# Optimization experiments

Measured on AMD Instinct MI355X. Metric: run time of the kernel, lower is better.

Reference implementation:

```python
import jax, jax.numpy as jnp
import numpy as np

GROUP = 16   # self.group
K = 3        # self.k (top-3 motif rows)


def _unfold3(x):
    # nn.Unfold(kernel_size=3): [B,C,H,W] -> [B, C*9, (H-2)*(W-2)]
    # torch channel ordering: c-major, then kernel offsets row-major.
    B, C, H, W = x.shape
    Ho, Wo = H - 2, W - 2
    pats = jnp.stack([x[:, :, i:i + Ho, j:j + Wo]
                      for i in range(3) for j in range(3)], axis=2)  # [B,C,9,Ho,Wo]
    return pats.reshape(B, C * 9, Ho * Wo)


def _fold3(y, H, W):
    # nn.Fold(output_size=(H,W), kernel_size=3): sum overlapping patches back.
    B, C9, L = y.shape
    C = C9 // 9
    Ho, Wo = H - 2, W - 2
    y = y.reshape(B, C, 3, 3, Ho, Wo)
    out = jnp.zeros((B, C, H, W), y.dtype)
    for i in range(3):
        for j in range(3):
            out = out.at[:, :, i:i + Ho, j:j + Wo].add(y[:, :, i, j])
    return out


def _group_motif(xg, H, W):
    motif = _unfold3(xg)                                  # [B,P,L], P = Cg*9
    B, P, L = motif.shape
    # torch.cdist (p=2) between the P rows, via the Gram trick.
    sq = jnp.sum(motif * motif, axis=-1)                  # [B,P]
    gram = jnp.einsum('bpl,bql->bpq', motif, motif)       # [B,P,P]
    d2 = sq[:, :, None] + sq[:, None, :] - 2.0 * gram
    dist = jnp.sqrt(jnp.maximum(d2, 0.0))
    eye = jnp.eye(P, dtype=bool)[None]
    dist = jnp.where(eye, jnp.inf, dist)                  # diagonal := inf
    # topk(k=1, largest=False) == argmin over last dim
    min_idx = jnp.argmin(dist, axis=-1)                   # [B,P] int
    # torch.unique(return_counts=True) over the whole tensor (flattened over batch)
    counts = jnp.bincount(min_idx.ravel(), length=P)      # [P] int
    # sort counts descending, take first K uniques -> lax.top_k
    top_c, top_i = jax.lax.top_k(counts, K)               # [K],[K]
    total = jnp.sum(top_c).astype(motif.dtype)
    rows = motif[:, top_i, :]                             # [B,K,L] gathered motif rows
    cf = top_c.astype(motif.dtype)
    motif_new = jnp.zeros_like(motif)
    for o in range(K):
        # torch: motif * motif[:, u_o].unsqueeze(1) * c_o // total  (floor division)
        motif_new = motif_new + jnp.floor(motif * rows[:, o][:, None, :] * cf[o] / total)
    return _fold3(motif_new, H, W)


def setup_inputs() -> dict:
    key = jax.random.key(0)
    feature = jax.random.normal(key, (2, 256, 192, 192), dtype=jnp.float32)
    return {"feature": feature}


def reference(feature):
    B, C, H, W = feature.shape
    chunks = jnp.split(feature, GROUP, axis=1)
    outs = [_group_motif(g, H, W) for g in chunks]
    return jnp.concatenate(outs, axis=1)                  # [B, C, H, W]
```

## Files before the change

kernel.cpp:

```cpp
#include <hip/hip_runtime.h>
#include <math.h>

#define NB 2
#define NC 256
#define CG 16
#define HH 192
#define WW 192
#define HO 190
#define PP 144

typedef float v2f __attribute__((ext_vector_type(2)));

#define SMEM_FLOATS 7348

#define GLD16(GP, LP)                                                         \
    __builtin_amdgcn_global_load_lds(                                         \
        (const __attribute__((address_space(1))) void*)(GP),                  \
        (__attribute__((address_space(3))) void*)(LP), 16, 0, 0)

__global__ __launch_bounds__(192, 2) void gram_kernel(const float* __restrict__ x,
                                                      double* __restrict__ gram)
{
    __shared__ __align__(16) float smem[SMEM_FLOATS];
    float* const red_s = smem + 2548;

    const int v = threadIdx.x;
    const int p = v & 1;
    const int bb = (v + 2) & ~1;

    const int bid = blockIdx.x;
    const int vx = bid & 7;
    const int tq = bid >> 3;
    const int idxw = tq / 36;
    const int rr0 = tq - idxw * 36;
    const int hg = idxw * 8 + vx;
    const int bg = hg >> 1;
    int r = rr0 + 36 * (hg & 1);
    int c2 = 0;
    while (r >= (c2 + 2) / 2) { r -= (c2 + 2) / 2; ++c2; }
    const int c1a = 2 * r;
    int c1b = 2 * r + 1;
    const bool bval = (c1b <= c2);
    if (!bval) c1b = c2;
    const int b = bg >> 4, g = bg & 15;

    const float* __restrict__ xa  = x + ((size_t)(b * NC + g * CG + c1a)) * (HH * WW);
    const float* __restrict__ xb  = x + ((size_t)(b * NC + g * CG + c1b)) * (HH * WW);
    const float* __restrict__ x2g = x + ((size_t)(b * NC + g * CG + c2 )) * (HH * WW);

    v2f midA[15], midB[15];
#pragma unroll
    for (int o = 0; o < 15; ++o) { midA[o] = (v2f){0.f, 0.f}; midB[o] = (v2f){0.f, 0.f}; }

    v2f win[6][3];
    float ca[6], cb[6];
#pragma unroll
    for (int k = 0; k < 6; ++k) {
        ca[k] = xa[(size_t)(2 + k) * WW + v];
        cb[k] = xb[(size_t)(2 + k) * WW + v];
    }

    const float* pa = xa + (size_t)8 * WW + v;
    const float* pb = xb + (size_t)8 * WW + v;
    int lds_off;

#define USTEP6(P, WPF, GPF)                                                   \
    {                                                                         \
        const float a1 = ca[(P)];                                             \
        const float b1 = cb[(P)];                                             \
        if (GPF) { ca[(P)] = pa[(P) * WW]; cb[(P)] = pb[(P) * WW]; }          \
        if (WPF) {                                                            \
            _Pragma("unroll")                                                 \
            for (int pr = 0; pr < 3; ++pr)                                    \
                win[((P) + 5) % 6][pr] = *(const v2f*)(&smem[lds_off + 2 * pr]); \
        }                                                                     \
        lds_off += 196;                                                       \
        const v2f a2 = (v2f){a1, a1};                                         \
        const v2f b2 = (v2f){b1, b1};                                         \
        _Pragma("unroll")                                                     \
        for (int kk = 0; kk < 5; ++kk) {                                      \
            _Pragma("unroll")                                                 \
            for (int pr = 0; pr < 3; ++pr) {                                  \
                const v2f wv = win[((P) + kk) % 6][pr];                       \
                midA[kk * 3 + pr] = __builtin_elementwise_fma(a2, wv, midA[kk * 3 + pr]); \
                midB[kk * 3 + pr] = __builtin_elementwise_fma(b2, wv, midB[kk * 3 + pr]); \
            }                                                                 \
        }                                                                     \
    }

#define STAGE(ROW0, NROUND, LASTN)                                            \
    __syncthreads();                                                          \
    _Pragma("unroll")                                                         \
    for (int rr2 = 0; rr2 < (NROUND); ++rr2) {                                \
        if (rr2 < (NROUND) - 1 || v < (LASTN)) {                              \
            const int slot = rr2 * 192 + v;                                   \
            const int row = slot / 49;                                        \
            const int s49 = slot - row * 49;                                  \
            const int col = (s49 == 0) ? 0 : (s49 - 1) * 4;                   \
            const float* gp2 = x2g + (size_t)((ROW0) + row) * WW + col;       \
            float* lp = smem + (rr2 * 192 + (v & ~63)) * 4;                   \
            GLD16(gp2, lp);                                                   \
        }                                                                     \
    }                                                                         \
    __syncthreads();                                                          \
    if (v < 144) smem[(v >> 2) * 196 + (v & 3)] = 0.f;                        \
    __syncthreads();

    for (int band = 0; band < 6; ++band) {
        const int row0 = band * 30;
        STAGE(row0, 9, 179)

        if (band == 0) {
#pragma unroll
            for (int k = 0; k < 5; ++k)
#pragma unroll
            for (int pr = 0; pr < 3; ++pr)
                win[k][pr] = *(const v2f*)(&smem[k * 196 + bb + 2 * pr]);
        }

        lds_off = 5 * 196 + bb;
        for (int it = 0; it < 5; ++it) {
            USTEP6(0, 1, 1) USTEP6(1, 1, 1) USTEP6(2, 1, 1)
            USTEP6(3, 1, 1) USTEP6(4, 1, 1) USTEP6(5, 1, 1)
            pa += 6 * WW; pb += 6 * WW;
        }
    }
    STAGE(180, 4, 12)
    lds_off = 5 * 196 + bb;
    USTEP6(0, 1, 1) USTEP6(1, 1, 1) USTEP6(2, 1, 0)
    USTEP6(3, 1, 0) USTEP6(4, 1, 0) USTEP6(5, 1, 0)
    USTEP6(0, 1, 0) USTEP6(1, 0, 0)
#undef USTEP6
#undef STAGE

    __syncthreads();
    for (int i = 0; i < 12; ++i) {
        const int ar = (i < 6) ? (i - 2) : (188 + i - 6);
        const float val = (ar >= 0 && ar <= 191) ? x2g[(size_t)ar * WW + v] : 0.f;
        smem[i * 196 + 4 + v] = val;
    }
    __syncthreads();

    double* const gp = gram + (size_t)bg * (PP * PP);

#pragma unroll
    for (int i1 = 0; i1 < 3; ++i1) {
        const int ra = (i1 == 0) ? 0 : ((i1 == 1) ? 1 : 190);
        const int rb = (i1 == 0) ? 1 : ((i1 == 1) ? 190 : 191);
#pragma unroll
        for (int c = 0; c < 2; ++c) {
            const float* __restrict__ xc = (c == 0) ? xa : xb;
            const float xra = xc[(size_t)ra * WW + v];
            const float xrb = xc[(size_t)rb * WW + v];
#pragma unroll
            for (int k = 0; k < 5; ++k) {
                const int bufa = (ra < 2) ? (ra + k) : (ra + k - 184);
                const int bufb = (rb < 2) ? (rb + k) : (rb + k - 184);
#pragma unroll
                for (int dj = 0; dj < 5; ++dj) {
                    float ve, vo;
                    {
                        const int pr = dj >> 1, ln = dj & 1;
                        const v2f m = (c == 0) ? midA[k * 3 + pr] : midB[k * 3 + pr];
                        ve = ln ? m.y : m.x;
                    }
                    {
                        const int pr = (dj + 1) >> 1, ln = (dj + 1) & 1;
                        const v2f m = (c == 0) ? midA[k * 3 + pr] : midB[k * 3 + pr];
                        vo = ln ? m.y : m.x;
                    }
                    float cw = p ? vo : ve;
                    cw = fmaf(xra, smem[bufa * 196 + 2 + v + dj], cw);
                    cw = fmaf(xrb, smem[bufb * 196 + 2 + v + dj], cw);
                    red_s[v * 25 + k * 5 + dj] = cw;
                }
            }
            __syncthreads();
            float e0 = 0.f, e1 = 0.f, e190 = 0.f, e191 = 0.f;
            if (v < 25) {
                e0   = red_s[0 * 25 + v];
                e1   = red_s[1 * 25 + v];
                e190 = red_s[190 * 25 + v];
                e191 = red_s[191 * 25 + v];
            }
            __syncthreads();
#pragma unroll
            for (int s = 96; s >= 3; s >>= 1) {
                for (int idx = v; idx < s * 25; idx += 192) {
                    const int vv = idx / 25, o = idx - vv * 25;
                    red_s[vv * 25 + o] += red_s[(vv + s) * 25 + o];
                }
                __syncthreads();
            }
            if (v < 25 && (c == 0 || bval)) {
                const int di = v / 5 - 2, dj = v - (v / 5) * 5 - 2;
                const int i2 = i1 + di;
                if (i2 >= 0 && i2 <= 2) {
                    const float S = red_s[0 * 25 + v] + red_s[1 * 25 + v] + red_s[2 * 25 + v];
                    const int c1 = (c == 0) ? c1a : c1b;
#pragma unroll
                    for (int j1 = 0; j1 < 3; ++j1) {
                        const int j2 = j1 + dj;
                        if (j2 < 0 || j2 > 2) continue;
                        const float W = S - ((j1 == 0) ? (e190 + e191)
                                          : (j1 == 1) ? (e0 + e191)
                                                      : (e0 + e1));
                        const int pp = c1 * 9 + i1 * 3 + j1;
                        const int qq = c2 * 9 + i2 * 3 + j2;
                        gp[pp * PP + qq] = (double)W;
                        if (c1 != c2) gp[qq * PP + pp] = (double)W;
                    }
                }
            }
            __syncthreads();
        }
    }
}

__global__ __launch_bounds__(320) void topk_kernel(const double* __restrict__ gram,
                                                   float* __restrict__ pf,
                                                   int* __restrict__ pi)
{
    const int g = blockIdx.x;
    __shared__ double sdiag[2][PP];
    __shared__ int counts[PP];
    const int tid = threadIdx.x;
    if (tid < PP) counts[tid] = 0;
    if (tid < 2 * PP) {
        const int b = tid / PP, p = tid % PP;
        const double* gb = gram + (size_t)(b * 16 + g) * (PP * PP);
        sdiag[b][p] = gb[p * PP + p];
    }
    __syncthreads();
    if (tid < 2 * PP) {
        const int b = tid / PP, p = tid % PP;
        const double* row = gram + ((size_t)(b * 16 + g) * PP + p) * PP;
        const double sp = sdiag[b][p];
        double best = 1e300;
        int bi = 0;
        for (int q = 0; q < PP; ++q) {
            if (q == p) continue;
            const double d2 = sp + sdiag[b][q] - 2.0 * row[q];
            if (d2 < best) { best = d2; bi = q; }
        }
        atomicAdd(&counts[bi], 1);
    }
    __syncthreads();
    if (tid == 0) {
        int sel[3], cv[3];
        for (int o = 0; o < 3; ++o) {
            int bc = -1, bp = 0;
            for (int p = 0; p < PP; ++p) {
                bool taken = false;
                for (int u = 0; u < o; ++u) if (sel[u] == p) taken = true;
                if (!taken && counts[p] > bc) { bc = counts[p]; bp = p; }
            }
            sel[o] = bp; cv[o] = bc;
        }
        const int tot = cv[0] + cv[1] + cv[2];
        for (int o = 0; o < 3; ++o) {
            pf[g * 4 + o] = (float)cv[o];
            pi[g * 4 + o] = sel[o];
        }
        pf[g * 4 + 3] = (float)tot;
    }
}

template <bool EDGE>
__device__ __forceinline__ void motif_quad(const float* __restrict__ x,
                                           const float* __restrict__ pf,
                                           const int* __restrict__ pi,
                                           float* __restrict__ out,
                                           int b, int ch, int h, int w0)
{
    const int g = ch >> 4;
    const size_t base = ((size_t)(b * NC + ch)) * (HH * WW);
    const float4 xv4 = *(const float4*)(x + base + (size_t)h * WW + w0);
    const float xs[4] = {xv4.x, xv4.y, xv4.z, xv4.w};
    float acc[4] = {0.f, 0.f, 0.f, 0.f};
    const float total = pf[g * 4 + 3];
    const double invd = 1.0 / (double)total;

#pragma unroll
    for (int o = 0; o < 3; ++o) {
        const int p = pi[g * 4 + o];
        const float cff = pf[g * 4 + o];
        const int co = p / 9;
        const int kk = p - co * 9;
        const int io = kk / 3, jo = kk - (kk / 3) * 3;
        const float* Rb = x + ((size_t)(b * NC + g * CG + co)) * (HH * WW);
#pragma unroll
        for (int i = 0; i < 3; ++i) {
            const int ho = h - i;
            bool rowok = true;
            int hr = ho + io;
            if (EDGE) {
                rowok = (ho >= 0) && (ho < HO);
                hr = hr < 0 ? 0 : (hr > HH - 1 ? HH - 1 : hr);
            }
            const float* row = Rb + (size_t)hr * WW;
            float rv[6];
#pragma unroll
            for (int u = 0; u < 6; ++u) {
                int col = w0 - 2 + jo + u;
                if (EDGE) col = col < 0 ? 0 : (col > WW - 1 ? WW - 1 : col);
                rv[u] = row[col];
            }
#pragma unroll
            for (int j = 0; j < 3; ++j)
#pragma unroll
            for (int q = 0; q < 4; ++q) {
                const float r2 = rv[q - j + 2];
                const float t1 = xs[q] * r2;
                const float t2 = t1 * cff;
                const float qf = (float)((double)t2 * invd);
                const float vfl = floorf(qf);
                if (EDGE) {
                    const int wo = w0 + q - j;
                    const bool ok = rowok && (wo >= 0) && (wo < HO);
                    acc[q] += ok ? vfl : 0.f;
                } else {
                    acc[q] += vfl;
                }
            }
        }
    }
    float4 ov = make_float4(acc[0], acc[1], acc[2], acc[3]);
    *(float4*)(out + base + (size_t)h * WW + w0) = ov;
}

__global__ __launch_bounds__(256) void out_interior(const float* __restrict__ x,
                                                    const float* __restrict__ pf,
                                                    const int* __restrict__ pi,
                                                    float* __restrict__ out)
{
    const int gid = blockIdx.x * 256 + threadIdx.x;
    const int w4i = gid % 46;
    int t = gid / 46;
    const int h = 2 + t % 188; t /= 188;
    const int ch = t & 255;
    const int b = t >> 8;
    motif_quad<false>(x, pf, pi, out, b, ch, h, (w4i + 1) * 4);
}

__global__ __launch_bounds__(256) void out_edge(const float* __restrict__ x,
                                                const float* __restrict__ pf,
                                                const int* __restrict__ pi,
                                                float* __restrict__ out)
{
    const int gid = blockIdx.x * 256 + threadIdx.x;
    const int e = gid % 568;
    int t = gid / 568;
    const int ch = t & 255;
    const int b = t >> 8;
    int h, w4;
    if (e < 192) {
        const int hs = e / 48;
        h = (hs < 2) ? hs : 188 + hs;
        w4 = e % 48;
    } else {
        const int e2 = e - 192;
        h = 2 + (e2 >> 1);
        w4 = (e2 & 1) ? 47 : 0;
    }
    motif_quad<true>(x, pf, pi, out, b, ch, h, w4 * 4);
}

extern "C" void kernel_launch(void* const* d_in, const int* in_sizes, int n_in,
                              void* d_out, int out_size, void* d_ws, size_t ws_size,
                              hipStream_t stream)
{
    const float* x = (const float*)d_in[0];
    float* out = (float*)d_out;

    double* gram = (double*)d_ws;
    const size_t gram_bytes = (size_t)32 * PP * PP * sizeof(double);
    float* pf = (float*)((char*)d_ws + gram_bytes);
    int* pi = (int*)((char*)d_ws + gram_bytes + 256);

    gram_kernel<<<2304, 192, 0, stream>>>(x, gram);
    topk_kernel<<<16, 320, 0, stream>>>(gram, pf, pi);
    out_interior<<<17296, 256, 0, stream>>>(x, pf, pi, out);
    out_edge<<<1136, 256, 0, stream>>>(x, pf, pi, out);
}
```

Baseline: 364.1 us.

## Shrink gram LDS footprint, fold reduction, merge output kernels, float-divide via FMA refinement

The gram kernel stages smaller 24-row bands so its LDS buffer is smaller, and pre-folds the 192-entry epilogue reduction into 96 slots with edge values kept in a separate small buffer. The aim is to let more blocks fit per CU and cut one reduction round. The two output kernels are merged into a single launch, and the double-precision divide is replaced by a float reciprocal with one FMA correction step. That change risks floor() results differing from the exact division in rare cases.

```diff
diff --git a/kernel.cpp b/kernel.cpp
--- a/kernel.cpp
+++ b/kernel.cpp
@@ -11,7 +11,7 @@
 
 typedef float v2f __attribute__((ext_vector_type(2)));
 
-#define SMEM_FLOATS 7348
+#define SMEM_FLOATS 5684
 
 #define GLD16(GP, LP)                                                         \
     __builtin_amdgcn_global_load_lds(                                         \
@@ -22,7 +22,8 @@
                                                       double* __restrict__ gram)
 {
     __shared__ __align__(16) float smem[SMEM_FLOATS];
-    float* const red_s = smem + 2548;
+    float* const red2 = smem + 2548;
+    float* const ebuf = smem + 4948;
 
     const int v = threadIdx.x;
     const int p = v & 1;
@@ -103,12 +104,11 @@
         }                                                                     \
     }                                                                         \
     __syncthreads();                                                          \
-    if (v < 144) smem[(v >> 2) * 196 + (v & 3)] = 0.f;                        \
+    if (v < 116) smem[(v >> 2) * 196 + (v & 3)] = 0.f;                        \
     __syncthreads();
 
-    for (int band = 0; band < 6; ++band) {
-        const int row0 = band * 30;
-        STAGE(row0, 9, 179)
+    for (int band = 0; band < 7; ++band) {
+        STAGE(band * 24, 8, 77)
 
         if (band == 0) {
 #pragma unroll
@@ -119,14 +119,20 @@
         }
 
         lds_off = 5 * 196 + bb;
-        for (int it = 0; it < 5; ++it) {
+        for (int it = 0; it < 4; ++it) {
             USTEP6(0, 1, 1) USTEP6(1, 1, 1) USTEP6(2, 1, 1)
             USTEP6(3, 1, 1) USTEP6(4, 1, 1) USTEP6(5, 1, 1)
             pa += 6 * WW; pb += 6 * WW;
         }
     }
-    STAGE(180, 4, 12)
+    STAGE(168, 7, 24)
     lds_off = 5 * 196 + bb;
+    USTEP6(0, 1, 1) USTEP6(1, 1, 1) USTEP6(2, 1, 1)
+    USTEP6(3, 1, 1) USTEP6(4, 1, 1) USTEP6(5, 1, 1)
+    pa += 6 * WW; pb += 6 * WW;
+    USTEP6(0, 1, 1) USTEP6(1, 1, 1) USTEP6(2, 1, 1)
+    USTEP6(3, 1, 1) USTEP6(4, 1, 1) USTEP6(5, 1, 1)
+    pa += 6 * WW; pb += 6 * WW;
     USTEP6(0, 1, 1) USTEP6(1, 1, 1) USTEP6(2, 1, 0)
     USTEP6(3, 1, 0) USTEP6(4, 1, 0) USTEP6(5, 1, 0)
     USTEP6(0, 1, 0) USTEP6(1, 0, 0)
@@ -143,6 +149,21 @@
 
     double* const gp = gram + (size_t)bg * (PP * PP);
 
+#define EPI_CW(KQ, DJ, CVAL)                                                  \
+    ({                                                                        \
+        float ve_, vo_;                                                       \
+        { const int pr_ = (DJ) >> 1, ln_ = (DJ) & 1;                          \
+          const v2f m_ = ((CVAL) == 0) ? midA[(KQ) * 3 + pr_] : midB[(KQ) * 3 + pr_]; \
+          ve_ = ln_ ? m_.y : m_.x; }                                          \
+        { const int pr_ = ((DJ) + 1) >> 1, ln_ = ((DJ) + 1) & 1;              \
+          const v2f m_ = ((CVAL) == 0) ? midA[(KQ) * 3 + pr_] : midB[(KQ) * 3 + pr_]; \
+          vo_ = ln_ ? m_.y : m_.x; }                                          \
+        float cw_ = p ? vo_ : ve_;                                            \
+        cw_ = fmaf(xra, smem[bufa * 196 + 2 + v + (DJ)], cw_);                \
+        cw_ = fmaf(xrb, smem[bufb * 196 + 2 + v + (DJ)], cw_);                \
+        cw_;                                                                  \
+    })
+
 #pragma unroll
     for (int i1 = 0; i1 < 3; ++i1) {
         const int ra = (i1 == 0) ? 0 : ((i1 == 1) ? 1 : 190);
@@ -152,43 +173,50 @@
             const float* __restrict__ xc = (c == 0) ? xa : xb;
             const float xra = xc[(size_t)ra * WW + v];
             const float xrb = xc[(size_t)rb * WW + v];
-#pragma unroll
-            for (int k = 0; k < 5; ++k) {
-                const int bufa = (ra < 2) ? (ra + k) : (ra + k - 184);
-                const int bufb = (rb < 2) ? (rb + k) : (rb + k - 184);
-#pragma unroll
-                for (int dj = 0; dj < 5; ++dj) {
-                    float ve, vo;
-                    {
-                        const int pr = dj >> 1, ln = dj & 1;
-                        const v2f m = (c == 0) ? midA[k * 3 + pr] : midB[k * 3 + pr];
-                        ve = ln ? m.y : m.x;
-                    }
-                    {
-                        const int pr = (dj + 1) >> 1, ln = (dj + 1) & 1;
-                        const v2f m = (c == 0) ? midA[k * 3 + pr] : midB[k * 3 + pr];
-                        vo = ln ? m.y : m.x;
-                    }
-                    float cw = p ? vo : ve;
-                    cw = fmaf(xra, smem[bufa * 196 + 2 + v + dj], cw);
-                    cw = fmaf(xrb, smem[bufb * 196 + 2 + v + dj], cw);
-                    red_s[v * 25 + k * 5 + dj] = cw;
+            if (v >= 96) {
+#pragma unroll
+                for (int k = 0; k < 5; ++k) {
+                    const int bufa = (ra < 2) ? (ra + k) : (ra + k - 184);
+                    const int bufb = (rb < 2) ? (rb + k) : (rb + k - 184);
+#pragma unroll
+                    for (int dj = 0; dj < 5; ++dj)
+                        red2[(v - 96) * 25 + k * 5 + dj] = EPI_CW(k, dj, c);
+                }
+            } else if (v < 2) {
+#pragma unroll
+                for (int k = 0; k < 5; ++k) {
+                    const int bufa = (ra < 2) ? (ra + k) : (ra + k - 184);
+                    const int bufb = (rb < 2) ? (rb + k) : (rb + k - 184);
+#pragma unroll
+                    for (int dj = 0; dj < 5; ++dj)
+                        ebuf[v * 25 + k * 5 + dj] = EPI_CW(k, dj, c);
                 }
             }
             __syncthreads();
             float e0 = 0.f, e1 = 0.f, e190 = 0.f, e191 = 0.f;
             if (v < 25) {
-                e0   = red_s[0 * 25 + v];
-                e1   = red_s[1 * 25 + v];
-                e190 = red_s[190 * 25 + v];
-                e191 = red_s[191 * 25 + v];
+                e0   = ebuf[v];
+                e1   = ebuf[25 + v];
+                e190 = red2[94 * 25 + v];
+                e191 = red2[95 * 25 + v];
             }
             __syncthreads();
-#pragma unroll
-            for (int s = 96; s >= 3; s >>= 1) {
+            if (v < 96) {
+#pragma unroll
+                for (int k = 0; k < 5; ++k) {
+                    const int bufa = (ra < 2) ? (ra + k) : (ra + k - 184);
+                    const int bufb = (rb < 2) ? (rb + k) : (rb + k - 184);
+#pragma unroll
+                    for (int dj = 0; dj < 5; ++dj)
+                        red2[v * 25 + k * 5 + dj] += EPI_CW(k, dj, c);
+                }
+            }
+            __syncthreads();
+#pragma unroll
+            for (int s = 48; s >= 3; s >>= 1) {
                 for (int idx = v; idx < s * 25; idx += 192) {
                     const int vv = idx / 25, o = idx - vv * 25;
-                    red_s[vv * 25 + o] += red_s[(vv + s) * 25 + o];
+                    red2[vv * 25 + o] += red2[(vv + s) * 25 + o];
                 }
                 __syncthreads();
             }
@@ -196,7 +224,7 @@
                 const int di = v / 5 - 2, dj = v - (v / 5) * 5 - 2;
                 const int i2 = i1 + di;
                 if (i2 >= 0 && i2 <= 2) {
-                    const float S = red_s[0 * 25 + v] + red_s[1 * 25 + v] + red_s[2 * 25 + v];
+                    const float S = red2[0 * 25 + v] + red2[1 * 25 + v] + red2[2 * 25 + v];
                     const int c1 = (c == 0) ? c1a : c1b;
 #pragma unroll
                     for (int j1 = 0; j1 < 3; ++j1) {
@@ -215,6 +243,7 @@
             __syncthreads();
         }
     }
+#undef EPI_CW
 }
 
 __global__ __launch_bounds__(320) void topk_kernel(const double* __restrict__ gram,
@@ -279,7 +308,7 @@
     const float xs[4] = {xv4.x, xv4.y, xv4.z, xv4.w};
     float acc[4] = {0.f, 0.f, 0.f, 0.f};
     const float total = pf[g * 4 + 3];
-    const double invd = 1.0 / (double)total;
+    const float rcp = (float)(1.0 / (double)total);
 
 #pragma unroll
     for (int o = 0; o < 3; ++o) {
@@ -313,7 +342,9 @@
                 const float r2 = rv[q - j + 2];
                 const float t1 = xs[q] * r2;
                 const float t2 = t1 * cff;
-                const float qf = (float)((double)t2 * invd);
+                const float q0 = t2 * rcp;
+                const float rr = fmaf(-total, q0, t2);
+                const float qf = fmaf(rr, rcp, q0);
                 const float vfl = floorf(qf);
                 if (EDGE) {
                     const int wo = w0 + q - j;
@@ -329,41 +360,41 @@
     *(float4*)(out + base + (size_t)h * WW + w0) = ov;
 }
 
-__global__ __launch_bounds__(256) void out_interior(const float* __restrict__ x,
-                                                    const float* __restrict__ pf,
-                                                    const int* __restrict__ pi,
-                                                    float* __restrict__ out)
+#define NBLK_INT 17296
+#define NBLK_EDGE 1136
+
+__global__ __launch_bounds__(256) void out_kernel(const float* __restrict__ x,
+                                                  const float* __restrict__ pf,
+                                                  const int* __restrict__ pi,
+                                                  float* __restrict__ out)
 {
-    const int gid = blockIdx.x * 256 + threadIdx.x;
-    const int w4i = gid % 46;
-    int t = gid / 46;
-    const int h = 2 + t % 188; t /= 188;
-    const int ch = t & 255;
-    const int b = t >> 8;
-    motif_quad<false>(x, pf, pi, out, b, ch, h, (w4i + 1) * 4);
-}
-
-__global__ __launch_bounds__(256) void out_edge(const float* __restrict__ x,
-                                                const float* __restrict__ pf,
-                                                const int* __restrict__ pi,
-                                                float* __restrict__ out)
-{
-    const int gid = blockIdx.x * 256 + threadIdx.x;
-    const int e = gid % 568;
-    int t = gid / 568;
-    const int ch = t & 255;
-    const int b = t >> 8;
-    int h, w4;
-    if (e < 192) {
-        const int hs = e / 48;
-        h = (hs < 2) ? hs : 188 + hs;
-        w4 = e % 48;
+    const int bid = blockIdx.x;
+    if (bid < NBLK_INT) {
+        const int gid = bid * 256 + threadIdx.x;
+        const int w4i = gid % 46;
+        int t = gid / 46;
+        const int h = 2 + t % 188; t /= 188;
+        const int ch = t & 255;
+        const int b = t >> 8;
+        motif_quad<false>(x, pf, pi, out, b, ch, h, (w4i + 1) * 4);
     } else {
-        const int e2 = e - 192;
-        h = 2 + (e2 >> 1);
-        w4 = (e2 & 1) ? 47 : 0;
-    }
-    motif_quad<true>(x, pf, pi, out, b, ch, h, w4 * 4);
+        const int gid = (bid - NBLK_INT) * 256 + threadIdx.x;
+        const int e = gid % 568;
+        int t = gid / 568;
+        const int ch = t & 255;
+        const int b = t >> 8;
+        int h, w4;
+        if (e < 192) {
+            const int hs = e / 48;
+            h = (hs < 2) ? hs : 188 + hs;
+            w4 = e % 48;
+        } else {
+            const int e2 = e - 192;
+            h = 2 + (e2 >> 1);
+            w4 = (e2 & 1) ? 47 : 0;
+        }
+        motif_quad<true>(x, pf, pi, out, b, ch, h, w4 * 4);
+    }
 }
 
 extern "C" void kernel_launch(void* const* d_in, const int* in_sizes, int n_in,
@@ -380,6 +411,5 @@
 
     gram_kernel<<<2304, 192, 0, stream>>>(x, gram);
     topk_kernel<<<16, 320, 0, stream>>>(gram, pf, pi);
-    out_interior<<<17296, 256, 0, stream>>>(x, pf, pi, out);
-    out_edge<<<1136, 256, 0, stream>>>(x, pf, pi, out);
+    out_kernel<<<NBLK_INT + NBLK_EDGE, 256, 0, stream>>>(x, pf, pi, out);
 }
```

Result: faster. 351.2 us (median of 2 runs) (-3.5%).
